# Optimization experiments

Measured on AMD Instinct MI355X. Metric: run time of the kernel, lower is better.

Reference implementation:

```python
import jax
import jax.numpy as jnp
import numpy as np

B, C, H, W = 32, 192, 28, 28
OUT, K, GROUPS = 384, 9, 4


def setup_inputs() -> dict:
    key = jax.random.key(0)
    k1, k2, k3 = jax.random.split(key, 3)
    x = jax.random.normal(k1, (B, C, H, W), dtype=jnp.float32)
    # 1x1 grouped conv (groups=4): weight [out_channels, in_channels*2 // groups]
    weight = jax.random.normal(k2, (OUT, 2 * C // GROUPS), dtype=jnp.float32) * 0.05
    bias = jax.random.normal(k3, (OUT,), dtype=jnp.float32) * 0.05
    return {"x": x, "weight": weight, "bias": bias}


def _knn_indices(xf, k):
    """xf: [B, C, N] node features. Returns nn_idx [B, N, k] (no grad)."""
    xf = jax.lax.stop_gradient(xf)
    # L2-normalize along channel dim (F.normalize p=2 dim=1, eps=1e-12)
    nrm = jnp.sqrt(jnp.sum(xf * xf, axis=1, keepdims=True))
    xn = xf / jnp.maximum(nrm, 1e-12)
    pts = jnp.transpose(xn, (0, 2, 1))  # [B, N, C]
    sq = jnp.sum(pts * pts, axis=-1)  # [B, N]
    # dist = ||x_i||^2 - 2 x_i.y_j + ||y_j||^2
    dist = sq[:, :, None] - 2.0 * jnp.einsum("bnc,bmc->bnm", pts, pts) + sq[:, None, :]
    _, nn_idx = jax.lax.top_k(-dist, k)  # smallest distances -> [B, N, k]
    return nn_idx


def reference(x, weight, bias):
    b, c, h, w = x.shape
    n = h * w
    xf = x.reshape(b, c, n)  # [B, C, N]

    nn_idx = _knn_indices(xf, K)  # [B, N, K]

    feat = jnp.transpose(xf, (0, 2, 1))  # [B, N, C]
    # gather neighbor features: x_j [B, C, N, K]
    x_j = jax.vmap(lambda f, i: f[i])(feat, nn_idx)  # [B, N, K, C]
    x_j = jnp.transpose(x_j, (0, 3, 1, 2))  # [B, C, N, K]
    x_i = xf[:, :, :, None]  # [B, C, N, 1] (center = identity gather)

    # EdgeConv features: cat([x_i, x_j - x_i]) -> [B, 2C, N, K]
    edge = jnp.concatenate(
        [jnp.broadcast_to(x_i, x_j.shape), x_j - x_i], axis=1
    )

    # 1x1 grouped conv (groups=4) + bias + exact GELU
    cin_g = 2 * c // GROUPS
    cout_g = OUT // GROUPS
    eg = edge.reshape(b, GROUPS, cin_g, n, K)
    wg = weight.reshape(GROUPS, cout_g, cin_g)
    y = jnp.einsum("bgcnk,goc->bgonk", eg, wg).reshape(b, OUT, n, K)
    y = y + bias[None, :, None, None]
    y = jax.nn.gelu(y, approximate=False)

    # max over neighbors
    y = jnp.max(y, axis=-1)  # [B, OUT, N]
    return y.reshape(b, OUT, h, w)
```

## Files before the change

### kernel.cpp

```cpp
#include <hip/hip_runtime.h>
#include <math.h>

#define BSZ 32
#define CCH 192
#define NPIX 784
#define NP 896
#define NGRP 56
#define NGU 49
#define OUTC 384
#define KNN 9

typedef short s8v __attribute__((ext_vector_type(8)));
typedef float f4v __attribute__((ext_vector_type(4)));

#define XFH_BYTES ((size_t)BSZ * NGRP * 6 * 64 * 8 * 2)
#define XFL_BYTES XFH_BYTES
#define PAIR_BYTES ((size_t)BSZ * NP * 8)
#define IDX_BYTES ((size_t)BSZ * NPIX * KNN * 4)
#define TBUF_BYTES ((size_t)BSZ * 192 * NPIX * 4)
#define WF_BYTES ((size_t)24 * 3 * 64 * 8 * 2)

__device__ __forceinline__ ushort bf16_rne(float f) {
    uint u = __float_as_uint(f);
    uint r = (u + 0x7fffu + ((u >> 16) & 1u)) >> 16;
    return (ushort)r;
}
__device__ __forceinline__ float bf16f(ushort h) { return __uint_as_float(((uint)h) << 16); }

__device__ __forceinline__ float gelu_fast(float u) {
    float x = u * 0.70710678118654752440f;
    float ax = fabsf(x);
    float t = __builtin_amdgcn_rcpf(fmaf(0.3275911f, ax, 1.0f));
    float p = t * fmaf(t, fmaf(t, fmaf(t, fmaf(t, 1.061405429f, -1.453152027f),
                                       1.421413741f), -0.284496736f), 0.254829592f);
    float e = __expf(-ax * ax);
    float erf_ax = fmaf(-p, e, 1.0f);
    float erfx = copysignf(erf_ax, x);
    return 0.5f * u * (1.0f + erfx);
}

__global__ __launch_bounds__(64) void k0_wfrag(const float* __restrict__ w,
                                               ushort* __restrict__ wfh,
                                               ushort* __restrict__ wfl) {
    int c2 = blockIdx.x;
    int l = threadIdx.x;
    int ob = c2 / 3, kc = c2 - ob * 3;
    int row = ob * 16 + (l & 15);
    int k0c = kc * 32 + (l >> 4) * 8;
    const float* wr = w + row * 96 + k0c;
    s8v hv, lv;
#pragma unroll
    for (int k = 0; k < 8; ++k) {
        float v = wr[k];
        ushort h = bf16_rne(v);
        hv[k] = (short)h;
        lv[k] = (short)bf16_rne(v - bf16f(h));
    }
    *(s8v*)(wfh + ((size_t)c2 * 64 + l) * 8) = hv;
    *(s8v*)(wfl + ((size_t)c2 * 64 + l) * 8) = lv;
}

__global__ __launch_bounds__(256) void k1_normalize(const float* __restrict__ x,
                                                    ushort* __restrict__ xfh,
                                                    ushort* __restrict__ xfl,
                                                    float2* __restrict__ pair) {
    __shared__ float xs[CCH][65];
    int b = blockIdx.y;
    int n0 = blockIdx.x * 64;
    int t = threadIdx.x;
    const float* xb = x + (size_t)b * CCH * NPIX;

    for (int i = t; i < CCH * 64; i += 256) {
        int c = i >> 6, j = i & 63, n = n0 + j;
        xs[c][j] = (n < NPIX) ? xb[c * NPIX + n] : 0.f;
    }
    __syncthreads();

    {
        int j = t >> 2, part = t & 3;
        float ss = 0.f;
        for (int k = 0; k < 48; ++k) { float v = xs[part * 48 + k][j]; ss = fmaf(v, v, ss); }
        ss += __shfl_xor(ss, 1);
        ss += __shfl_xor(ss, 2);
        float inv = 1.0f / fmaxf(sqrtf(ss), 1e-12f);
        float s2 = 0.f;
        for (int k = 0; k < 48; ++k) {
            float v = xs[part * 48 + k][j] * inv;
            s2 = fmaf(v, v, s2);
        }
        s2 += __shfl_xor(s2, 1);
        s2 += __shfl_xor(s2, 2);
        if (part == 0) {
            int n = n0 + j;
            pair[b * NP + n] = (n < NPIX) ? make_float2(s2, inv) : make_float2(1e30f, 0.f);
        }
    }

#pragma unroll
    for (int i = 0; i < 6; ++i) {
        int ch = t + i * 256;
        int g = ch / 384, rem = ch - g * 384;
        int kc = rem >> 6, l = rem & 63;
        int nl = g * 16 + (l & 15);
        int c0 = kc * 32 + (l >> 4) * 8;
        s8v hv, lv;
#pragma unroll
        for (int k = 0; k < 8; ++k) {
            float v = xs[c0 + k][nl];
            ushort h = bf16_rne(v);
            hv[k] = (short)h;
            lv[k] = (short)bf16_rne(v - bf16f(h));
        }
        size_t doff = (((size_t)(b * NGRP + (n0 >> 4) + g)) * 6 + kc) * 512 + (size_t)l * 8;
        *(s8v*)(xfh + doff) = hv;
        *(s8v*)(xfl + doff) = lv;
    }
}

__device__ __forceinline__ bool lt_pair(float v, int id, float dv, int di) {
    return (v < dv) || (v == dv && id < di);
}
__device__ __forceinline__ void ins9b(float (&d)[KNN], int (&ii)[KNN], float v, int id) {
    bool c[KNN];
#pragma unroll
    for (int p = 0; p < KNN; ++p) c[p] = v < d[p];
    float nd[KNN]; int ni[KNN];
    nd[0] = c[0] ? v : d[0];
    ni[0] = c[0] ? id : ii[0];
#pragma unroll
    for (int p = 1; p < KNN; ++p) {
        nd[p] = c[p - 1] ? d[p - 1] : (c[p] ? v : d[p]);
        ni[p] = c[p - 1] ? ii[p - 1] : (c[p] ? id : ii[p]);
    }
#pragma unroll
    for (int p = 0; p < KNN; ++p) { d[p] = nd[p]; ii[p] = ni[p]; }
}

__global__ __launch_bounds__(128) void k2_knn(const ushort* __restrict__ xfh,
                                              const ushort* __restrict__ xfl,
                                              const float* __restrict__ pair,
                                              int* __restrict__ nnidx) {
    __shared__ ushort qlds[12 * 512];
    __shared__ float dls[2][64][KNN];
    __shared__ int   ils[2][64][KNN];
    int wg = blockIdx.x;
    int b  = (wg & 7) * 4 + (wg >> 3) / 49;
    int qt = (wg >> 3) % 49;
    int t = threadIdx.x, w = t >> 6, l = t & 63;
    int lk = l >> 4;
    const ushort* fh = xfh + (size_t)b * NGRP * 3072;
    const ushort* fl = xfl + (size_t)b * NGRP * 3072;
    const float2* pb = (const float2*)(pair + (size_t)b * NP * 2);
    int l8 = l * 8;

    {
        const ushort* qh_g = fh + (size_t)qt * 3072;
        const ushort* ql_g = fl + (size_t)qt * 3072;
        for (int i = t; i < 768; i += 128) {
            int half = i / 384;
            int off = (i - half * 384) * 8;
            s8v v = *(const s8v*)((half ? ql_g : qh_g) + off);
            *(s8v*)(qlds + half * 3072 + off) = v;
        }
    }
    float c2q = -2.f * pb[qt * 16 + (l & 15)].y;
    __syncthreads();

    float d9[KNN]; int i9[KNN];
#pragma unroll
    for (int r = 0; r < KNN; ++r) { d9[r] = 3.4e38f; i9[r] = 0x7fffffff; }

    const ushort* qp = qlds + l8;

    int g0 = w ? 24 : 0, g1 = w ? NGU : 24;
#pragma unroll 2
    for (int cg = g0; cg < g1; ++cg) {
        const ushort* ch = fh + (size_t)cg * 3072 + l8;
        const ushort* cl = fl + (size_t)cg * 3072 + l8;
        f4v aH  = {0.f, 0.f, 0.f, 0.f};
        f4v aX1 = {0.f, 0.f, 0.f, 0.f};
        f4v aX2 = {0.f, 0.f, 0.f, 0.f};
        f4v aX3 = {0.f, 0.f, 0.f, 0.f};
#pragma unroll
        for (int kc = 0; kc < 6; ++kc) {
            s8v vh = *(const s8v*)(ch + kc * 512);
            s8v vl = *(const s8v*)(cl + kc * 512);
            s8v qh = *(const s8v*)(qp + kc * 512);
            s8v ql = *(const s8v*)(qp + 3072 + kc * 512);
            aH  = __builtin_amdgcn_mfma_f32_16x16x32_bf16(vh, qh, aH,  0, 0, 0);
            aX1 = __builtin_amdgcn_mfma_f32_16x16x32_bf16(vl, qh, aX1, 0, 0, 0);
            aX2 = __builtin_amdgcn_mfma_f32_16x16x32_bf16(vh, ql, aX2, 0, 0, 0);
            aX3 = __builtin_amdgcn_mfma_f32_16x16x32_bf16(vl, ql, aX3, 0, 0, 0);
        }
        float4 pA = *(const float4*)(pb + (size_t)(cg * 16 + lk * 4));
        float4 pB = *(const float4*)(pb + (size_t)(cg * 16 + lk * 4) + 2);
        float sqn_[4] = {pA.x, pA.z, pB.x, pB.z};
        float inv_[4] = {pA.y, pA.w, pB.y, pB.w};
#pragma unroll
        for (int r = 0; r < 4; ++r) {
            float v = fmaf(c2q * inv_[r], aH[r] + aX1[r] + aX2[r] + aX3[r], sqn_[r]);
            ins9b(d9, i9, v, cg * 16 + lk * 4 + r);
        }
    }

#pragma unroll
    for (int r = 0; r < KNN; ++r) { dls[w][l][r] = d9[r]; ils[w][l][r] = i9[r]; }
    __syncthreads();
    if (t < 16) {
        int q = qt * 16 + t;
        int pk[8] = {0, 0, 0, 0, 0, 0, 0, 0};
        int* op = nnidx + ((size_t)b * NPIX + q) * KNN;
        for (int r = 0; r < KNN; ++r) {
            float best = 3.4e38f; int bi = 0x7fffffff; int bk = 0;
#pragma unroll
            for (int m = 0; m < 8; ++m) {
                int ww = m >> 2, kk = m & 3;
                int idx = pk[m] < KNN ? pk[m] : KNN - 1;
                float v = dls[ww][kk * 16 + t][idx];
                int ii = ils[ww][kk * 16 + t][idx];
                if (pk[m] < KNN && lt_pair(v, ii, best, bi)) { best = v; bi = ii; bk = m; }
            }
            op[r] = bi;
#pragma unroll
            for (int m = 0; m < 8; ++m) pk[m] += (m == bk) ? 1 : 0;
        }
    }
}

__global__ __launch_bounds__(256, 2) void k3_proj(const ushort* __restrict__ xfh,
                                                  const ushort* __restrict__ xfl,
                                                  const ushort* __restrict__ wfh,
                                                  const ushort* __restrict__ wfl,
                                                  const float* __restrict__ bias,
                                                  float* __restrict__ out,
                                                  float* __restrict__ tbuf) {
    int wg = blockIdx.x;
    int b  = (wg & 7) * 4 + (wg >> 3) / 49;
    int ng = (wg >> 3) % 49;
    int t = threadIdx.x, g = t >> 6, l = t & 63;
    int h = l >> 4, m16 = l & 15;
    int kb = (g & 1) * 3;
    int l8 = l * 8;

    const ushort* fh = xfh + (((size_t)(b * NGRP + ng)) * 6 + kb) * 512 + l8;
    const ushort* fl = xfl + (((size_t)(b * NGRP + ng)) * 6 + kb) * 512 + l8;
    s8v xh[3], xl[3];
#pragma unroll
    for (int kk = 0; kk < 3; ++kk) {
        xh[kk] = *(const s8v*)(fh + kk * 512);
        xl[kk] = *(const s8v*)(fl + kk * 512);
    }

    for (int ogg = 0; ogg < 6; ++ogg) {
        int ob = g * 6 + ogg;
        const ushort* ph = wfh + ((size_t)ob * 3) * 512 + l8;
        const ushort* pl = wfl + ((size_t)ob * 3) * 512 + l8;
        f4v acc = {0.f, 0.f, 0.f, 0.f};
#pragma unroll
        for (int kk = 0; kk < 3; ++kk) {
            s8v wh = *(const s8v*)(ph + kk * 512);
            s8v wl = *(const s8v*)(pl + kk * 512);
            acc = __builtin_amdgcn_mfma_f32_16x16x32_bf16(xh[kk], wh, acc, 0, 0, 0);
            acc = __builtin_amdgcn_mfma_f32_16x16x32_bf16(xh[kk], wl, acc, 0, 0, 0);
            acc = __builtin_amdgcn_mfma_f32_16x16x32_bf16(xl[kk], wh, acc, 0, 0, 0);
        }
        int row = g * 96 + ogg * 16 + m16;
        if (g < 2) {
            float bv = bias[row];
#pragma unroll
            for (int r = 0; r < 4; ++r) {
                int n = ng * 16 + h * 4 + r;
                out[((size_t)b * OUTC + row) * NPIX + n] = gelu_fast(acc[r] + bv);
            }
        } else {
            int r2 = (g - 2) * 96 + ogg * 16 + m16;
#pragma unroll
            for (int r = 0; r < 4; ++r) {
                int n = ng * 16 + h * 4 + r;
                tbuf[((size_t)b * 192 + r2) * NPIX + n] = acc[r];
            }
        }
    }
}

__global__ __launch_bounds__(256) void k4_gather(const float* __restrict__ tbuf,
                                                 const int* __restrict__ nnidx,
                                                 const float* __restrict__ bias,
                                                 float* __restrict__ out) {
    __shared__ float trow[NPIX];
    __shared__ int nn[NPIX * KNN];
    int wg = blockIdx.x;
    int b   = (wg & 7) * 4 + (wg >> 3) / 24;
    int oct = (wg >> 3) % 24;
    int t = threadIdx.x;
    const int4* nb4 = (const int4*)(nnidx + (size_t)b * NPIX * KNN);
    for (int i = t; i < NPIX * KNN / 4; i += 256) ((int4*)nn)[i] = nb4[i];

    for (int oo = 0; oo < 8; ++oo) {
        int og2 = oct * 8 + oo;
        const float4* tr4 = (const float4*)(tbuf + ((size_t)b * 192 + og2) * NPIX);
        for (int i = t; i < NPIX / 4; i += 256) ((float4*)trow)[i] = tr4[i];
        __syncthreads();
        float bv = bias[192 + og2];
        float* orow = out + ((size_t)b * OUTC + 192 + og2) * NPIX;
        for (int n = t; n < NPIX; n += 256) {
            float ti = trow[n];
            const int* ip = nn + n * KNN;
            float umin = 3.4e38f, umax = -3.4e38f;
#pragma unroll
            for (int k = 0; k < KNN; ++k) {
                int j = ip[k];
                float u = trow[j] - ti + bv;
                umin = fminf(umin, u);
                umax = fmaxf(umax, u);
            }
            orow[n] = fmaxf(gelu_fast(umin), gelu_fast(umax));
        }
        __syncthreads();
    }
}

extern "C" void kernel_launch(void* const* d_in, const int* in_sizes, int n_in,
                              void* d_out, int out_size, void* d_ws, size_t ws_size,
                              hipStream_t stream) {
    const float* x    = (const float*)d_in[0];
    const float* w    = (const float*)d_in[1];
    const float* bias = (const float*)d_in[2];
    float* out = (float*)d_out;
    char* ws = (char*)d_ws;

    ushort* xfh   = (ushort*)(ws);
    ushort* xfl   = (ushort*)(ws + XFH_BYTES);
    float2* pair  = (float2*)(ws + XFH_BYTES + XFL_BYTES);
    int*    nnidx = (int*)   (ws + XFH_BYTES + XFL_BYTES + PAIR_BYTES);
    float*  tbuf  = (float*) (ws + XFH_BYTES + XFL_BYTES + PAIR_BYTES + IDX_BYTES);
    ushort* wfh   = (ushort*)(ws + XFH_BYTES + XFL_BYTES + PAIR_BYTES + IDX_BYTES + TBUF_BYTES);
    ushort* wfl   = (ushort*)(ws + XFH_BYTES + XFL_BYTES + PAIR_BYTES + IDX_BYTES + TBUF_BYTES + WF_BYTES);

    k0_wfrag<<<dim3(72), 64, 0, stream>>>(w, wfh, wfl);
    k1_normalize<<<dim3(13, BSZ), 256, 0, stream>>>(x, xfh, xfl, pair);
    k2_knn<<<dim3(1568), 128, 0, stream>>>(xfh, xfl, (const float*)pair, nnidx);
    k3_proj<<<dim3(1568), 256, 0, stream>>>(xfh, xfl, wfh, wfl, bias, out, tbuf);
    k4_gather<<<dim3(768), 256, 0, stream>>>(tbuf, nnidx, bias, out);
}
```

Measured before the change: 133.6 us.

## Replace per-candidate top-9 insertion with med3 threshold filter and batched LDS insertion

Each candidate distance now goes through a value-only sorting network built from fmed3, which tracks a running 9th-smallest threshold. Only candidates at or below that threshold are staged in LDS. The staged candidates are merged into the index-tracked top-9 list in batches whenever any lane has nine or more pending, using an early-exit, index-aware insertion. This removes the full 9-slot select chain for distance plus index on every candidate. The cost is extra LDS traffic, a wavefront-divergent flush loop, and reuse of the shared buffer for the final merge.

```diff
diff --git a/kernel.cpp b/kernel.cpp
--- a/kernel.cpp
+++ b/kernel.cpp
@@ -120,20 +120,16 @@
 __device__ __forceinline__ bool lt_pair(float v, int id, float dv, int di) {
     return (v < dv) || (v == dv && id < di);
 }
-__device__ __forceinline__ void ins9b(float (&d)[KNN], int (&ii)[KNN], float v, int id) {
-    bool c[KNN];
-#pragma unroll
-    for (int p = 0; p < KNN; ++p) c[p] = v < d[p];
-    float nd[KNN]; int ni[KNN];
-    nd[0] = c[0] ? v : d[0];
-    ni[0] = c[0] ? id : ii[0];
-#pragma unroll
-    for (int p = 1; p < KNN; ++p) {
-        nd[p] = c[p - 1] ? d[p - 1] : (c[p] ? v : d[p]);
-        ni[p] = c[p - 1] ? ii[p - 1] : (c[p] ? id : ii[p]);
-    }
-#pragma unroll
-    for (int p = 0; p < KNN; ++p) { d[p] = nd[p]; ii[p] = ni[p]; }
+__device__ __forceinline__ void ins9p(float (&d)[KNN], int (&ii)[KNN], float v, int id) {
+    if (!lt_pair(v, id, d[KNN - 1], ii[KNN - 1])) return;
+    bool cprev = true;
+#pragma unroll
+    for (int p = KNN - 1; p >= 0; --p) {
+        bool cp = (p == 0) ? false : lt_pair(v, id, d[p - 1], ii[p - 1]);
+        float nd = cp ? d[p - 1] : (cprev ? v : d[p]);
+        int nid = cp ? ii[p - 1] : (cprev ? id : ii[p]);
+        d[p] = nd; ii[p] = nid; cprev = cp;
+    }
 }
 
 __global__ __launch_bounds__(128) void k2_knn(const ushort* __restrict__ xfh,
@@ -141,8 +137,7 @@
                                               const float* __restrict__ pair,
                                               int* __restrict__ nnidx) {
     __shared__ ushort qlds[12 * 512];
-    __shared__ float dls[2][64][KNN];
-    __shared__ int   ils[2][64][KNN];
+    __shared__ unsigned long long sk[12][128];
     int wg = blockIdx.x;
     int b  = (wg & 7) * 4 + (wg >> 3) / 49;
     int qt = (wg >> 3) % 49;
@@ -169,6 +164,9 @@
     float d9[KNN]; int i9[KNN];
 #pragma unroll
     for (int r = 0; r < KNN; ++r) { d9[r] = 3.4e38f; i9[r] = 0x7fffffff; }
+    float d0 = 3.4e38f, d1 = 3.4e38f, d2 = 3.4e38f, d3 = 3.4e38f, d4 = 3.4e38f,
+          d5 = 3.4e38f, d6 = 3.4e38f, d7 = 3.4e38f, d8 = 3.4e38f;
+    uint cnt = 0;
 
     const ushort* qp = qlds + l8;
 
@@ -199,12 +197,50 @@
 #pragma unroll
         for (int r = 0; r < 4; ++r) {
             float v = fmaf(c2q * inv_[r], aH[r] + aX1[r] + aX2[r] + aX3[r], sqn_[r]);
-            ins9b(d9, i9, v, cg * 16 + lk * 4 + r);
-        }
-    }
-
-#pragma unroll
-    for (int r = 0; r < KNN; ++r) { dls[w][l][r] = d9[r]; ils[w][l][r] = i9[r]; }
+            d8 = __builtin_amdgcn_fmed3f(v, d7, d8);
+            d7 = __builtin_amdgcn_fmed3f(v, d6, d7);
+            d6 = __builtin_amdgcn_fmed3f(v, d5, d6);
+            d5 = __builtin_amdgcn_fmed3f(v, d4, d5);
+            d4 = __builtin_amdgcn_fmed3f(v, d3, d4);
+            d3 = __builtin_amdgcn_fmed3f(v, d2, d3);
+            d2 = __builtin_amdgcn_fmed3f(v, d1, d2);
+            d1 = __builtin_amdgcn_fmed3f(v, d0, d1);
+            d0 = fminf(v, d0);
+            if (v <= d8) {
+                sk[cnt][t] = ((unsigned long long)__float_as_uint(v) << 32)
+                             | (uint)(cg * 16 + lk * 4 + r);
+                ++cnt;
+            }
+        }
+        if (__any((int)(cnt >= 9u))) {
+#pragma unroll 1
+            for (int j = 0; j < 12; ++j) {
+                if (!__any((int)((uint)j < cnt))) break;
+                if ((uint)j < cnt) {
+                    unsigned long long pv = sk[j][t];
+                    ins9p(d9, i9, __uint_as_float((uint)(pv >> 32)), (int)(uint)(pv & 0xffffffffu));
+                }
+            }
+            cnt = 0;
+        }
+    }
+#pragma unroll 1
+    for (int j = 0; j < 12; ++j) {
+        if (!__any((int)((uint)j < cnt))) break;
+        if ((uint)j < cnt) {
+            unsigned long long pv = sk[j][t];
+            ins9p(d9, i9, __uint_as_float((uint)(pv >> 32)), (int)(uint)(pv & 0xffffffffu));
+        }
+    }
+    __syncthreads();
+
+    float* dls = (float*)&sk[0][0];
+    int*   ils = (int*)(dls + 2 * 64 * KNN);
+#pragma unroll
+    for (int r = 0; r < KNN; ++r) {
+        dls[(w * 64 + l) * KNN + r] = d9[r];
+        ils[(w * 64 + l) * KNN + r] = i9[r];
+    }
     __syncthreads();
     if (t < 16) {
         int q = qt * 16 + t;
@@ -216,8 +252,8 @@
             for (int m = 0; m < 8; ++m) {
                 int ww = m >> 2, kk = m & 3;
                 int idx = pk[m] < KNN ? pk[m] : KNN - 1;
-                float v = dls[ww][kk * 16 + t][idx];
-                int ii = ils[ww][kk * 16 + t][idx];
+                float v = dls[(ww * 64 + kk * 16 + t) * KNN + idx];
+                int ii = ils[(ww * 64 + kk * 16 + t) * KNN + idx];
                 if (pk[m] < KNN && lt_pair(v, ii, best, bi)) { best = v; bi = ii; bk = m; }
             }
             op[r] = bi;
```

After: 158.4 us. 1.19x slower.

## Fuse kNN and projection kernels, reusing query tile staged in LDS

Applied to the files above, without the earlier changes.

Merges the kNN kernel and the 1x1 projection kernel into one launch that shares a block mapping (batch, 16-pixel tile). The projection reads the hi/lo bf16 features from the query tile already staged in LDS, so it no longer reloads them from global memory. With 128 threads per block, each wave now handles two output-channel groups serially. This saves one launch and the repeated feature reads, but projection work per block is now done by half as many threads, and it runs after the serial kNN merge, which may lengthen the critical path.

```diff
diff --git a/kernel.cpp b/kernel.cpp
--- a/kernel.cpp
+++ b/kernel.cpp
@@ -136,10 +136,15 @@
     for (int p = 0; p < KNN; ++p) { d[p] = nd[p]; ii[p] = ni[p]; }
 }
 
-__global__ __launch_bounds__(128) void k2_knn(const ushort* __restrict__ xfh,
-                                              const ushort* __restrict__ xfl,
-                                              const float* __restrict__ pair,
-                                              int* __restrict__ nnidx) {
+__global__ __launch_bounds__(128) void k23_knn_proj(const ushort* __restrict__ xfh,
+                                                    const ushort* __restrict__ xfl,
+                                                    const float* __restrict__ pair,
+                                                    const ushort* __restrict__ wfh,
+                                                    const ushort* __restrict__ wfl,
+                                                    const float* __restrict__ bias,
+                                                    int* __restrict__ nnidx,
+                                                    float* __restrict__ out,
+                                                    float* __restrict__ tbuf) {
     __shared__ ushort qlds[12 * 512];
     __shared__ float dls[2][64][KNN];
     __shared__ int   ils[2][64][KNN];
@@ -225,59 +230,47 @@
             for (int m = 0; m < 8; ++m) pk[m] += (m == bk) ? 1 : 0;
         }
     }
-}
-
-__global__ __launch_bounds__(256, 2) void k3_proj(const ushort* __restrict__ xfh,
-                                                  const ushort* __restrict__ xfl,
-                                                  const ushort* __restrict__ wfh,
-                                                  const ushort* __restrict__ wfl,
-                                                  const float* __restrict__ bias,
-                                                  float* __restrict__ out,
-                                                  float* __restrict__ tbuf) {
-    int wg = blockIdx.x;
-    int b  = (wg & 7) * 4 + (wg >> 3) / 49;
-    int ng = (wg >> 3) % 49;
-    int t = threadIdx.x, g = t >> 6, l = t & 63;
-    int h = l >> 4, m16 = l & 15;
-    int kb = (g & 1) * 3;
-    int l8 = l * 8;
-
-    const ushort* fh = xfh + (((size_t)(b * NGRP + ng)) * 6 + kb) * 512 + l8;
-    const ushort* fl = xfl + (((size_t)(b * NGRP + ng)) * 6 + kb) * 512 + l8;
-    s8v xh[3], xl[3];
-#pragma unroll
-    for (int kk = 0; kk < 3; ++kk) {
-        xh[kk] = *(const s8v*)(fh + kk * 512);
-        xl[kk] = *(const s8v*)(fl + kk * 512);
-    }
-
-    for (int ogg = 0; ogg < 6; ++ogg) {
-        int ob = g * 6 + ogg;
-        const ushort* ph = wfh + ((size_t)ob * 3) * 512 + l8;
-        const ushort* pl = wfl + ((size_t)ob * 3) * 512 + l8;
-        f4v acc = {0.f, 0.f, 0.f, 0.f};
-#pragma unroll
-        for (int kk = 0; kk < 3; ++kk) {
-            s8v wh = *(const s8v*)(ph + kk * 512);
-            s8v wl = *(const s8v*)(pl + kk * 512);
-            acc = __builtin_amdgcn_mfma_f32_16x16x32_bf16(xh[kk], wh, acc, 0, 0, 0);
-            acc = __builtin_amdgcn_mfma_f32_16x16x32_bf16(xh[kk], wl, acc, 0, 0, 0);
-            acc = __builtin_amdgcn_mfma_f32_16x16x32_bf16(xl[kk], wh, acc, 0, 0, 0);
-        }
-        int row = g * 96 + ogg * 16 + m16;
-        if (g < 2) {
-            float bv = bias[row];
-#pragma unroll
-            for (int r = 0; r < 4; ++r) {
-                int n = ng * 16 + h * 4 + r;
-                out[((size_t)b * OUTC + row) * NPIX + n] = gelu_fast(acc[r] + bv);
+
+    {
+        int h = l >> 4, m16 = l & 15;
+        for (int gg = 0; gg < 2; ++gg) {
+            int g = w * 2 + gg;
+            int kb = (g & 1) * 3;
+            s8v xh[3], xl[3];
+#pragma unroll
+            for (int kk = 0; kk < 3; ++kk) {
+                xh[kk] = *(const s8v*)(qlds + (kb + kk) * 512 + l8);
+                xl[kk] = *(const s8v*)(qlds + 3072 + (kb + kk) * 512 + l8);
             }
-        } else {
-            int r2 = (g - 2) * 96 + ogg * 16 + m16;
-#pragma unroll
-            for (int r = 0; r < 4; ++r) {
-                int n = ng * 16 + h * 4 + r;
-                tbuf[((size_t)b * 192 + r2) * NPIX + n] = acc[r];
+            for (int ogg = 0; ogg < 6; ++ogg) {
+                int ob = g * 6 + ogg;
+                const ushort* ph = wfh + ((size_t)ob * 3) * 512 + l8;
+                const ushort* pl = wfl + ((size_t)ob * 3) * 512 + l8;
+                f4v acc = {0.f, 0.f, 0.f, 0.f};
+#pragma unroll
+                for (int kk = 0; kk < 3; ++kk) {
+                    s8v wh_ = *(const s8v*)(ph + kk * 512);
+                    s8v wl_ = *(const s8v*)(pl + kk * 512);
+                    acc = __builtin_amdgcn_mfma_f32_16x16x32_bf16(xh[kk], wh_, acc, 0, 0, 0);
+                    acc = __builtin_amdgcn_mfma_f32_16x16x32_bf16(xh[kk], wl_, acc, 0, 0, 0);
+                    acc = __builtin_amdgcn_mfma_f32_16x16x32_bf16(xl[kk], wh_, acc, 0, 0, 0);
+                }
+                int row = g * 96 + ogg * 16 + m16;
+                if (g < 2) {
+                    float bv = bias[row];
+#pragma unroll
+                    for (int r = 0; r < 4; ++r) {
+                        int n = qt * 16 + h * 4 + r;
+                        out[((size_t)b * OUTC + row) * NPIX + n] = gelu_fast(acc[r] + bv);
+                    }
+                } else {
+                    int r2 = (g - 2) * 96 + ogg * 16 + m16;
+#pragma unroll
+                    for (int r = 0; r < 4; ++r) {
+                        int n = qt * 16 + h * 4 + r;
+                        tbuf[((size_t)b * 192 + r2) * NPIX + n] = acc[r];
+                    }
+                }
             }
         }
     }
@@ -339,7 +332,7 @@
 
     k0_wfrag<<<dim3(72), 64, 0, stream>>>(w, wfh, wfl);
     k1_normalize<<<dim3(13, BSZ), 256, 0, stream>>>(x, xfh, xfl, pair);
-    k2_knn<<<dim3(1568), 128, 0, stream>>>(xfh, xfl, (const float*)pair, nnidx);
-    k3_proj<<<dim3(1568), 256, 0, stream>>>(xfh, xfl, wfh, wfl, bias, out, tbuf);
+    k23_knn_proj<<<dim3(1568), 128, 0, stream>>>(xfh, xfl, (const float*)pair,
+                                                 wfh, wfl, bias, nnidx, out, tbuf);
     k4_gather<<<dim3(768), 256, 0, stream>>>(tbuf, nnidx, bias, out);
 }
```

After: 124.8 us. 6.5% less time.
